# Optimization experiments

Hardware: AMD Instinct MI355X
Metric: run time of the kernel (lower is better)

## Reference

```python
import jax, jax.numpy as jnp
import numpy as np


def setup_inputs() -> dict:
    key = jax.random.key(0)
    k1, k2, k3, k4 = jax.random.split(key, 4)
    E, A = 1024, 64
    embedded = jax.random.normal(k1, (4, 4096, E), dtype=jnp.float32)
    # nn.Linear(E, A, bias=False) weight has shape [A, E]; y = x @ W.T
    W_K = jax.random.normal(k2, (A, E), dtype=jnp.float32) * (E ** -0.5)
    W_Q = jax.random.normal(k3, (A, E), dtype=jnp.float32) * (E ** -0.5)
    W_V = jax.random.normal(k4, (A, E), dtype=jnp.float32) * (E ** -0.5)
    return {"embedded": embedded, "W_K": W_K, "W_Q": W_Q, "W_V": W_V}


def reference(embedded, W_K, W_Q, W_V):
    A = W_K.shape[0]
    K = jnp.einsum('bse,ae->bsa', embedded, W_K)
    Q = jnp.einsum('bse,ae->bsa', embedded, W_Q)
    V = jnp.einsum('bse,ae->bsa', embedded, W_V)
    scores = jnp.einsum('bqa,bka->bqk', Q, K) / jnp.sqrt(jnp.float32(A))
    S = K.shape[1]
    causal = jnp.tril(jnp.ones((S, S), dtype=bool))  # True = keep
    scores = jnp.where(causal[None, :, :], scores, -jnp.inf)
    attn = jax.nn.softmax(scores, axis=2)
    out = jnp.einsum('bqk,bka->bqa', attn, V)
    return jnp.round(out, decimals=4)
```

## Files before the change

kernel.cpp:

```cpp
#include <hip/hip_runtime.h>
#include <math.h>

#define B_DIM 4
#define S_DIM 4096
#define E_DIM 1024
#define A_DIM 64
#define M_TOT (B_DIM * S_DIM)

typedef __bf16 v8bf __attribute__((ext_vector_type(8)));
typedef __bf16 v4bf __attribute__((ext_vector_type(4)));
typedef float  v4f  __attribute__((ext_vector_type(4)));

__device__ __forceinline__ v4f mfma16(v8bf a, v8bf b, v4f c) {
    return __builtin_amdgcn_mfma_f32_16x16x32_bf16(a, b, c, 0, 0, 0);
}

__device__ __forceinline__ void lds_dma16(const void* g, void* l) {
    __builtin_amdgcn_global_load_lds(
        (const __attribute__((address_space(1))) unsigned int*)g,
        (__attribute__((address_space(3))) unsigned int*)l, 16, 0, 0);
}

__global__ __launch_bounds__(256) void wconv_kernel(
    const float* __restrict__ Wk, const float* __restrict__ Wq,
    const float* __restrict__ Wv, __bf16* __restrict__ Wb)
{
    const int i = blockIdx.x * 256 + threadIdx.x;
    const int w = i >> 14;
    const int off = (i & 16383) * 4;
    const float* s = ((w == 0) ? Wk : (w == 1) ? Wq : Wv) + off;
    float4 v = *(const float4*)s;
    v4bf o;
    o[0] = (__bf16)v.x; o[1] = (__bf16)v.y; o[2] = (__bf16)v.z; o[3] = (__bf16)v.w;
    *(v4bf*)(Wb + (size_t)w * 65536 + off) = o;
}

__global__ __launch_bounds__(256) void qkv_proj_mfma(
    const float* __restrict__ X,
    const __bf16* __restrict__ Wb,
    __bf16* __restrict__ Kb,
    __bf16* __restrict__ Qb,
    __bf16* __restrict__ Vt)
{
    const int r0   = blockIdx.x * 64;
    const int w    = threadIdx.x >> 6;
    const int lane = threadIdx.x & 63;
    const int L    = lane & 15;
    const int quad = lane >> 4;
    const int cbase = w * 48;

    __shared__ __align__(16) char smem[18432 + 49152];
    __bf16* Xs = (__bf16*)smem;
    __bf16* Bs = (__bf16*)(smem + 18432);
    float (*Tv)[65] = (float(*)[65])smem;

    v4f acc[4][3];
#pragma unroll
    for (int mi = 0; mi < 4; ++mi)
#pragma unroll
        for (int nt = 0; nt < 3; ++nt) acc[mi][nt] = (v4f){0.f, 0.f, 0.f, 0.f};

    const int brow_l  = lane >> 3;
    const int bchunk  = lane & 7;
    const int bgchunk = bchunk ^ brow_l;
    auto stageB = [&](int kc, int buf) {
#pragma unroll
        for (int j = 0; j < 6; ++j) {
            const int rowbase = w * 48 + j * 8;
            const __bf16* g = Wb + (size_t)(rowbase + brow_l) * E_DIM
                              + kc * 64 + bgchunk * 8;
            lds_dma16(g, Bs + buf * 12288 + rowbase * 64);
        }
    };

    const int xrow_i = (lane >> 4);
    const int xcol   = (lane & 15) * 4;
    float4 xr[4];
    auto loadX = [&](int kc) {
#pragma unroll
        for (int i = 0; i < 4; ++i) {
            const int row = i * 16 + w * 4 + xrow_i;
            xr[i] = *(const float4*)(X + (size_t)(r0 + row) * E_DIM + kc * 64 + xcol);
        }
    };
    auto flushX = [&](int buf) {
#pragma unroll
        for (int i = 0; i < 4; ++i) {
            const int row = i * 16 + w * 4 + xrow_i;
            v4bf o;
            o[0] = (__bf16)xr[i].x; o[1] = (__bf16)xr[i].y;
            o[2] = (__bf16)xr[i].z; o[3] = (__bf16)xr[i].w;
            *(v4bf*)(Xs + buf * 4608 + row * 72 + xcol) = o;
        }
    };

    stageB(0, 0);
    loadX(0);
    flushX(0);
    __syncthreads();

#pragma unroll 1
    for (int kc = 0; kc < 16; ++kc) {
        const int cur = kc & 1;
        if (kc < 15) {
            stageB(kc + 1, cur ^ 1);
            loadX(kc + 1);
        }
        v8bf afr[4][2];
#pragma unroll
        for (int mi = 0; mi < 4; ++mi)
#pragma unroll
            for (int ka = 0; ka < 2; ++ka)
                afr[mi][ka] = *(const v8bf*)(Xs + cur * 4608 +
                                (mi * 16 + L) * 72 + ka * 32 + quad * 8);
        v8bf bfr[3][2];
#pragma unroll
        for (int nt = 0; nt < 3; ++nt)
#pragma unroll
            for (int ka = 0; ka < 2; ++ka) {
                const int R = cbase + nt * 16 + L;
                const int slot = (ka * 4 + quad) ^ (R & 7);
                bfr[nt][ka] = *(const v8bf*)(Bs + cur * 12288 + R * 64 + slot * 8);
            }
#pragma unroll
        for (int mi = 0; mi < 4; ++mi)
#pragma unroll
            for (int nt = 0; nt < 3; ++nt)
#pragma unroll
                for (int ka = 0; ka < 2; ++ka)
                    acc[mi][nt] = mfma16(afr[mi][ka], bfr[nt][ka], acc[mi][nt]);

        if (kc < 15) flushX(cur ^ 1);
        __syncthreads();
    }

#pragma unroll
    for (int nt = 0; nt < 3; ++nt) {
        const int c0 = cbase + nt * 16;
        if (c0 < 64) {
#pragma unroll
            for (int mi = 0; mi < 4; ++mi)
#pragma unroll
                for (int r = 0; r < 4; ++r)
                    Kb[(size_t)(r0 + mi * 16 + quad * 4 + r) * A_DIM + c0 + L] =
                        (__bf16)acc[mi][nt][r];
        } else if (c0 < 128) {
#pragma unroll
            for (int mi = 0; mi < 4; ++mi)
#pragma unroll
                for (int r = 0; r < 4; ++r)
                    Qb[(size_t)(r0 + mi * 16 + quad * 4 + r) * A_DIM + (c0 - 64) + L] =
                        (__bf16)(acc[mi][nt][r] * 0.125f);
        } else {
#pragma unroll
            for (int mi = 0; mi < 4; ++mi)
#pragma unroll
                for (int r = 0; r < 4; ++r)
                    Tv[mi * 16 + quad * 4 + r][(c0 - 128) + L] = acc[mi][nt][r];
        }
    }
    __syncthreads();

    {
        const int batch = r0 >> 12;
        const int s0    = r0 & 4095;
        const int a     = threadIdx.x >> 2;
        const int part  = threadIdx.x & 3;
        __bf16* vrow = Vt + (size_t)(batch * 64 + a) * S_DIM + s0 + part * 16;
#pragma unroll
        for (int h = 0; h < 2; ++h) {
            v8bf pk;
#pragma unroll
            for (int j = 0; j < 8; ++j)
                pk[j] = (__bf16)Tv[part * 16 + h * 8 + j][a];
            *(v8bf*)(vrow + h * 8) = pk;
        }
    }
}

__global__ __launch_bounds__(512, 2) void attn_fused(
    const __bf16* __restrict__ Qb,
    const __bf16* __restrict__ Kb,
    const __bf16* __restrict__ Vt,
    float* __restrict__ out)
{
    const int b  = blockIdx.y;
    const int qt = blockIdx.x;

    const int w    = threadIdx.x >> 6;
    const int lane = threadIdx.x & 63;
    const int L    = lane & 15;
    const int quad = lane >> 4;

    __shared__ __align__(16) char smem[73728];
    __bf16 (*Pt)[64][72]   = (__bf16(*)[64][72])smem;
    float*  red_l          = (float*)smem;
    float (*red_o)[64][65] = (float(*)[64][65])(smem + 2048);
    float*  invs           = (float*)(smem + 2048 + 66560);

    v8bf qf[4][2];
#pragma unroll
    for (int ni = 0; ni < 4; ++ni)
#pragma unroll
        for (int ka = 0; ka < 2; ++ka)
            qf[ni][ka] = *(const v8bf*)(Qb +
                (size_t)(b * S_DIM + qt * 64 + ni * 16 + L) * A_DIM + ka * 32 + quad * 8);

    v4f acc_o[4][4];
#pragma unroll
    for (int i = 0; i < 4; ++i)
#pragma unroll
        for (int j = 0; j < 4; ++j) acc_o[i][j] = (v4f){0.f, 0.f, 0.f, 0.f};
    float lrun[4] = {0.f, 0.f, 0.f, 0.f};

    for (int kt = w; kt <= qt; kt += 8) {
        v8bf kf[4][2];
#pragma unroll
        for (int mi = 0; mi < 4; ++mi)
#pragma unroll
            for (int ka = 0; ka < 2; ++ka)
                kf[mi][ka] = *(const v8bf*)(Kb +
                    (size_t)(b * S_DIM + kt * 64 + mi * 16 + L) * A_DIM + ka * 32 + quad * 8);
        v8bf vf[4][2];
#pragma unroll
        for (int ma = 0; ma < 4; ++ma)
#pragma unroll
            for (int ki = 0; ki < 2; ++ki)
                vf[ma][ki] = *(const v8bf*)(Vt +
                    (size_t)(b * 64 + ma * 16 + L) * S_DIM + kt * 64 + ki * 32 + quad * 8);

        const bool diag = (kt == qt);

#pragma unroll
        for (int ni = 0; ni < 4; ++ni) {
            v4f s[4];
#pragma unroll
            for (int mi = 0; mi < 4; ++mi) s[mi] = (v4f){0.f, 0.f, 0.f, 0.f};
#pragma unroll
            for (int mi = 0; mi < 4; ++mi)
#pragma unroll
                for (int ka = 0; ka < 2; ++ka)
                    s[mi] = mfma16(kf[mi][ka], qf[ni][ka], s[mi]);

            float rs = 0.f;
#pragma unroll
            for (int mi = 0; mi < 4; ++mi) {
                v4bf p4;
#pragma unroll
                for (int r = 0; r < 4; ++r) {
                    const bool masked = diag && (mi * 16 + quad * 4 + r > ni * 16 + L);
                    const float p = masked ? 0.f : __expf(s[mi][r]);
                    rs += p;
                    p4[r] = (__bf16)p;
                }
                *(v4bf*)&Pt[w][ni * 16 + L][mi * 16 + quad * 4] = p4;
            }
            lrun[ni] += rs;
        }

        v8bf pf[4][2];
#pragma unroll
        for (int ni = 0; ni < 4; ++ni)
#pragma unroll
            for (int ki = 0; ki < 2; ++ki)
                pf[ni][ki] = *(const v8bf*)&Pt[w][ni * 16 + L][ki * 32 + quad * 8];
#pragma unroll
        for (int ma = 0; ma < 4; ++ma)
#pragma unroll
            for (int ni = 0; ni < 4; ++ni)
#pragma unroll
                for (int ki = 0; ki < 2; ++ki)
                    acc_o[ma][ni] = mfma16(vf[ma][ki], pf[ni][ki], acc_o[ma][ni]);
    }

#pragma unroll
    for (int ni = 0; ni < 4; ++ni) {
        lrun[ni] += __shfl_xor(lrun[ni], 16, 64);
        lrun[ni] += __shfl_xor(lrun[ni], 32, 64);
    }

    __syncthreads();

    if (quad == 0) {
#pragma unroll
        for (int ni = 0; ni < 4; ++ni)
            red_l[w * 64 + ni * 16 + L] = lrun[ni];
    }
    if (w >= 4) {
#pragma unroll
        for (int ma = 0; ma < 4; ++ma)
#pragma unroll
            for (int ni = 0; ni < 4; ++ni)
#pragma unroll
                for (int r = 0; r < 4; ++r)
                    red_o[w - 4][ma * 16 + quad * 4 + r][ni * 16 + L] = acc_o[ma][ni][r];
    }
    __syncthreads();

    if (w < 4) {
#pragma unroll
        for (int ma = 0; ma < 4; ++ma)
#pragma unroll
            for (int ni = 0; ni < 4; ++ni)
#pragma unroll
                for (int r = 0; r < 4; ++r)
                    acc_o[ma][ni][r] += red_o[w][ma * 16 + quad * 4 + r][ni * 16 + L];
    } else if (w == 4) {
        float d = 0.f;
#pragma unroll
        for (int c = 0; c < 8; ++c) d += red_l[c * 64 + lane];
        invs[lane] = 1.0f / d;
    }
    __syncthreads();

    if (w < 4) {
#pragma unroll
        for (int ma = 0; ma < 4; ++ma)
#pragma unroll
            for (int ni = 0; ni < 4; ++ni)
#pragma unroll
                for (int r = 0; r < 4; ++r)
                    red_o[w][ma * 16 + quad * 4 + r][ni * 16 + L] = acc_o[ma][ni][r];
    }
    __syncthreads();

    {
        const int q  = threadIdx.x >> 3;
        const int ac = (threadIdx.x & 7) << 3;
        const float sc = invs[q];
        float* dst = out + (size_t)(b * S_DIM + qt * 64 + q) * A_DIM + ac;
#pragma unroll
        for (int i4 = 0; i4 < 2; ++i4) {
            float vv[4];
#pragma unroll
            for (int j = 0; j < 4; ++j) {
                const int a = ac + i4 * 4 + j;
                vv[j] = sc * (red_o[0][a][q] + red_o[1][a][q]
                            + red_o[2][a][q] + red_o[3][a][q]);
            }
            *(float4*)(dst + i4 * 4) = make_float4(vv[0], vv[1], vv[2], vv[3]);
        }
    }
}

extern "C" void kernel_launch(void* const* d_in, const int* in_sizes, int n_in,
                              void* d_out, int out_size, void* d_ws, size_t ws_size,
                              hipStream_t stream)
{
    const float* X  = (const float*)d_in[0];
    const float* Wk = (const float*)d_in[1];
    const float* Wq = (const float*)d_in[2];
    const float* Wv = (const float*)d_in[3];
    float* out = (float*)d_out;

    __bf16* Kb = (__bf16*)d_ws;
    __bf16* Qb = Kb + (size_t)M_TOT * A_DIM;
    __bf16* Vt = Qb + (size_t)M_TOT * A_DIM;
    __bf16* Wb = Vt + (size_t)M_TOT * A_DIM;

    wconv_kernel<<<192, 256, 0, stream>>>(Wk, Wq, Wv, Wb);

    qkv_proj_mfma<<<256, 256, 0, stream>>>(X, Wb, Kb, Qb, Vt);

    dim3 g2(64, B_DIM), b2(512);
    attn_fused<<<g2, b2, 0, stream>>>(Qb, Kb, Vt, out);
}
```

Measured before the change: 146.2 us.

## Balance causal attention work by pairing half query tiles; deepen X prefetch

```diff
diff --git a/kernel.cpp b/kernel.cpp
--- a/kernel.cpp
+++ b/kernel.cpp
@@ -75,37 +75,36 @@
 
     const int xrow_i = (lane >> 4);
     const int xcol   = (lane & 15) * 4;
-    float4 xr[4];
-    auto loadX = [&](int kc) {
+    float4 xr[2][4];
+    auto loadX = [&](int kc, int set) {
 #pragma unroll
         for (int i = 0; i < 4; ++i) {
             const int row = i * 16 + w * 4 + xrow_i;
-            xr[i] = *(const float4*)(X + (size_t)(r0 + row) * E_DIM + kc * 64 + xcol);
+            xr[set][i] = *(const float4*)(X + (size_t)(r0 + row) * E_DIM + kc * 64 + xcol);
         }
     };
-    auto flushX = [&](int buf) {
+    auto flushX = [&](int set, int buf) {
 #pragma unroll
         for (int i = 0; i < 4; ++i) {
             const int row = i * 16 + w * 4 + xrow_i;
             v4bf o;
-            o[0] = (__bf16)xr[i].x; o[1] = (__bf16)xr[i].y;
-            o[2] = (__bf16)xr[i].z; o[3] = (__bf16)xr[i].w;
+            o[0] = (__bf16)xr[set][i].x; o[1] = (__bf16)xr[set][i].y;
+            o[2] = (__bf16)xr[set][i].z; o[3] = (__bf16)xr[set][i].w;
             *(v4bf*)(Xs + buf * 4608 + row * 72 + xcol) = o;
         }
     };
 
     stageB(0, 0);
-    loadX(0);
-    flushX(0);
+    loadX(0, 0);
+    loadX(1, 1);
+    flushX(0, 0);
     __syncthreads();
 
 #pragma unroll 1
     for (int kc = 0; kc < 16; ++kc) {
         const int cur = kc & 1;
-        if (kc < 15) {
-            stageB(kc + 1, cur ^ 1);
-            loadX(kc + 1);
-        }
+        if (kc < 15) stageB(kc + 1, cur ^ 1);
+        if (kc < 14) loadX(kc + 2, cur);
         v8bf afr[4][2];
 #pragma unroll
         for (int mi = 0; mi < 4; ++mi)
@@ -122,6 +121,7 @@
                 const int slot = (ka * 4 + quad) ^ (R & 7);
                 bfr[nt][ka] = *(const v8bf*)(Bs + cur * 12288 + R * 64 + slot * 8);
             }
+        if (kc < 15) flushX((kc + 1) & 1, cur ^ 1);
 #pragma unroll
         for (int mi = 0; mi < 4; ++mi)
 #pragma unroll
@@ -130,7 +130,6 @@
                 for (int ka = 0; ka < 2; ++ka)
                     acc[mi][nt] = mfma16(afr[mi][ka], bfr[nt][ka], acc[mi][nt]);
 
-        if (kc < 15) flushX(cur ^ 1);
         __syncthreads();
     }
 
@@ -184,163 +183,177 @@
     const __bf16* __restrict__ Vt,
     float* __restrict__ out)
 {
-    const int b  = blockIdx.y;
-    const int qt = blockIdx.x;
+    const int b = blockIdx.y;
+    const int p = blockIdx.x;
 
     const int w    = threadIdx.x >> 6;
     const int lane = threadIdx.x & 63;
     const int L    = lane & 15;
     const int quad = lane >> 4;
 
-    __shared__ __align__(16) char smem[73728];
-    __bf16 (*Pt)[64][72]   = (__bf16(*)[64][72])smem;
+    __shared__ __align__(16) char smem[36864];
+    __bf16 (*Pt)[32][72]   = (__bf16(*)[32][72])smem;
     float*  red_l          = (float*)smem;
-    float (*red_o)[64][65] = (float(*)[64][65])(smem + 2048);
-    float*  invs           = (float*)(smem + 2048 + 66560);
-
-    v8bf qf[4][2];
-#pragma unroll
-    for (int ni = 0; ni < 4; ++ni)
-#pragma unroll
-        for (int ka = 0; ka < 2; ++ka)
-            qf[ni][ka] = *(const v8bf*)(Qb +
-                (size_t)(b * S_DIM + qt * 64 + ni * 16 + L) * A_DIM + ka * 32 + quad * 8);
-
-    v4f acc_o[4][4];
-#pragma unroll
-    for (int i = 0; i < 4; ++i)
-#pragma unroll
-        for (int j = 0; j < 4; ++j) acc_o[i][j] = (v4f){0.f, 0.f, 0.f, 0.f};
-    float lrun[4] = {0.f, 0.f, 0.f, 0.f};
-
-    for (int kt = w; kt <= qt; kt += 8) {
-        v8bf kf[4][2];
-#pragma unroll
-        for (int mi = 0; mi < 4; ++mi)
+    float (*red_o)[64][33] = (float(*)[64][33])(smem + 1024);
+    float*  invs           = (float*)(smem + 34816);
+
+    auto phase = [&](int qt, int qoff) {
+        v8bf qf[2][2];
+#pragma unroll
+        for (int ni = 0; ni < 2; ++ni)
 #pragma unroll
             for (int ka = 0; ka < 2; ++ka)
-                kf[mi][ka] = *(const v8bf*)(Kb +
-                    (size_t)(b * S_DIM + kt * 64 + mi * 16 + L) * A_DIM + ka * 32 + quad * 8);
-        v8bf vf[4][2];
-#pragma unroll
-        for (int ma = 0; ma < 4; ++ma)
-#pragma unroll
-            for (int ki = 0; ki < 2; ++ki)
-                vf[ma][ki] = *(const v8bf*)(Vt +
-                    (size_t)(b * 64 + ma * 16 + L) * S_DIM + kt * 64 + ki * 32 + quad * 8);
-
-        const bool diag = (kt == qt);
-
-#pragma unroll
-        for (int ni = 0; ni < 4; ++ni) {
-            v4f s[4];
-#pragma unroll
-            for (int mi = 0; mi < 4; ++mi) s[mi] = (v4f){0.f, 0.f, 0.f, 0.f};
+                qf[ni][ka] = *(const v8bf*)(Qb +
+                    (size_t)(b * S_DIM + qt * 64 + qoff + ni * 16 + L) * A_DIM
+                    + ka * 32 + quad * 8);
+
+        v4f acc_o[4][2];
+#pragma unroll
+        for (int i = 0; i < 4; ++i)
+#pragma unroll
+            for (int j = 0; j < 2; ++j) acc_o[i][j] = (v4f){0.f, 0.f, 0.f, 0.f};
+        float lrun[2] = {0.f, 0.f};
+
+        for (int kt = w; kt <= qt; kt += 8) {
+            v8bf kf[4][2];
 #pragma unroll
             for (int mi = 0; mi < 4; ++mi)
 #pragma unroll
                 for (int ka = 0; ka < 2; ++ka)
-                    s[mi] = mfma16(kf[mi][ka], qf[ni][ka], s[mi]);
-
-            float rs = 0.f;
-#pragma unroll
-            for (int mi = 0; mi < 4; ++mi) {
-                v4bf p4;
-#pragma unroll
-                for (int r = 0; r < 4; ++r) {
-                    const bool masked = diag && (mi * 16 + quad * 4 + r > ni * 16 + L);
-                    const float p = masked ? 0.f : __expf(s[mi][r]);
-                    rs += p;
-                    p4[r] = (__bf16)p;
+                    kf[mi][ka] = *(const v8bf*)(Kb +
+                        (size_t)(b * S_DIM + kt * 64 + mi * 16 + L) * A_DIM
+                        + ka * 32 + quad * 8);
+            v8bf vf[4][2];
+#pragma unroll
+            for (int ma = 0; ma < 4; ++ma)
+#pragma unroll
+                for (int ki = 0; ki < 2; ++ki)
+                    vf[ma][ki] = *(const v8bf*)(Vt +
+                        (size_t)(b * 64 + ma * 16 + L) * S_DIM + kt * 64
+                        + ki * 32 + quad * 8);
+
+            const bool diag = (kt == qt);
+
+#pragma unroll
+            for (int ni = 0; ni < 2; ++ni) {
+                v4f s[4];
+#pragma unroll
+                for (int mi = 0; mi < 4; ++mi) s[mi] = (v4f){0.f, 0.f, 0.f, 0.f};
+                __builtin_amdgcn_s_setprio(1);
+#pragma unroll
+                for (int mi = 0; mi < 4; ++mi)
+#pragma unroll
+                    for (int ka = 0; ka < 2; ++ka)
+                        s[mi] = mfma16(kf[mi][ka], qf[ni][ka], s[mi]);
+                __builtin_amdgcn_s_setprio(0);
+
+                float rs = 0.f;
+#pragma unroll
+                for (int mi = 0; mi < 4; ++mi) {
+                    v4bf p4;
+#pragma unroll
+                    for (int r = 0; r < 4; ++r) {
+                        const bool masked =
+                            diag && (mi * 16 + quad * 4 + r > qoff + ni * 16 + L);
+                        const float pv = masked ? 0.f : __expf(s[mi][r]);
+                        rs += pv;
+                        p4[r] = (__bf16)pv;
+                    }
+                    *(v4bf*)&Pt[w][ni * 16 + L][mi * 16 + quad * 4] = p4;
                 }
-                *(v4bf*)&Pt[w][ni * 16 + L][mi * 16 + quad * 4] = p4;
+                lrun[ni] += rs;
             }
-            lrun[ni] += rs;
-        }
-
-        v8bf pf[4][2];
-#pragma unroll
-        for (int ni = 0; ni < 4; ++ni)
-#pragma unroll
-            for (int ki = 0; ki < 2; ++ki)
-                pf[ni][ki] = *(const v8bf*)&Pt[w][ni * 16 + L][ki * 32 + quad * 8];
-#pragma unroll
-        for (int ma = 0; ma < 4; ++ma)
-#pragma unroll
-            for (int ni = 0; ni < 4; ++ni)
+
+            v8bf pf[2][2];
+#pragma unroll
+            for (int ni = 0; ni < 2; ++ni)
 #pragma unroll
                 for (int ki = 0; ki < 2; ++ki)
-                    acc_o[ma][ni] = mfma16(vf[ma][ki], pf[ni][ki], acc_o[ma][ni]);
-    }
-
-#pragma unroll
-    for (int ni = 0; ni < 4; ++ni) {
-        lrun[ni] += __shfl_xor(lrun[ni], 16, 64);
-        lrun[ni] += __shfl_xor(lrun[ni], 32, 64);
-    }
-
-    __syncthreads();
-
-    if (quad == 0) {
-#pragma unroll
-        for (int ni = 0; ni < 4; ++ni)
-            red_l[w * 64 + ni * 16 + L] = lrun[ni];
-    }
-    if (w >= 4) {
-#pragma unroll
-        for (int ma = 0; ma < 4; ++ma)
-#pragma unroll
-            for (int ni = 0; ni < 4; ++ni)
-#pragma unroll
-                for (int r = 0; r < 4; ++r)
-                    red_o[w - 4][ma * 16 + quad * 4 + r][ni * 16 + L] = acc_o[ma][ni][r];
-    }
-    __syncthreads();
-
-    if (w < 4) {
-#pragma unroll
-        for (int ma = 0; ma < 4; ++ma)
-#pragma unroll
-            for (int ni = 0; ni < 4; ++ni)
-#pragma unroll
-                for (int r = 0; r < 4; ++r)
-                    acc_o[ma][ni][r] += red_o[w][ma * 16 + quad * 4 + r][ni * 16 + L];
-    } else if (w == 4) {
-        float d = 0.f;
-#pragma unroll
-        for (int c = 0; c < 8; ++c) d += red_l[c * 64 + lane];
-        invs[lane] = 1.0f / d;
-    }
-    __syncthreads();
-
-    if (w < 4) {
-#pragma unroll
-        for (int ma = 0; ma < 4; ++ma)
-#pragma unroll
-            for (int ni = 0; ni < 4; ++ni)
-#pragma unroll
-                for (int r = 0; r < 4; ++r)
-                    red_o[w][ma * 16 + quad * 4 + r][ni * 16 + L] = acc_o[ma][ni][r];
-    }
-    __syncthreads();
-
-    {
-        const int q  = threadIdx.x >> 3;
-        const int ac = (threadIdx.x & 7) << 3;
-        const float sc = invs[q];
-        float* dst = out + (size_t)(b * S_DIM + qt * 64 + q) * A_DIM + ac;
-#pragma unroll
-        for (int i4 = 0; i4 < 2; ++i4) {
+                    pf[ni][ki] = *(const v8bf*)&Pt[w][ni * 16 + L][ki * 32 + quad * 8];
+            __builtin_amdgcn_s_setprio(1);
+#pragma unroll
+            for (int ma = 0; ma < 4; ++ma)
+#pragma unroll
+                for (int ni = 0; ni < 2; ++ni)
+#pragma unroll
+                    for (int ki = 0; ki < 2; ++ki)
+                        acc_o[ma][ni] = mfma16(vf[ma][ki], pf[ni][ki], acc_o[ma][ni]);
+            __builtin_amdgcn_s_setprio(0);
+        }
+
+#pragma unroll
+        for (int ni = 0; ni < 2; ++ni) {
+            lrun[ni] += __shfl_xor(lrun[ni], 16, 64);
+            lrun[ni] += __shfl_xor(lrun[ni], 32, 64);
+        }
+
+        __syncthreads();
+
+        if (quad == 0) {
+#pragma unroll
+            for (int ni = 0; ni < 2; ++ni)
+                red_l[w * 32 + ni * 16 + L] = lrun[ni];
+        }
+        if (w >= 4) {
+#pragma unroll
+            for (int ma = 0; ma < 4; ++ma)
+#pragma unroll
+                for (int ni = 0; ni < 2; ++ni)
+#pragma unroll
+                    for (int r = 0; r < 4; ++r)
+                        red_o[w - 4][ma * 16 + quad * 4 + r][ni * 16 + L] =
+                            acc_o[ma][ni][r];
+        }
+        __syncthreads();
+
+        if (w < 4) {
+#pragma unroll
+            for (int ma = 0; ma < 4; ++ma)
+#pragma unroll
+                for (int ni = 0; ni < 2; ++ni)
+#pragma unroll
+                    for (int r = 0; r < 4; ++r)
+                        acc_o[ma][ni][r] +=
+                            red_o[w][ma * 16 + quad * 4 + r][ni * 16 + L];
+        } else if (w == 4 && lane < 32) {
+            float d = 0.f;
+#pragma unroll
+            for (int c = 0; c < 8; ++c) d += red_l[c * 32 + lane];
+            invs[lane] = 1.0f / d;
+        }
+        __syncthreads();
+
+        if (w < 4) {
+#pragma unroll
+            for (int ma = 0; ma < 4; ++ma)
+#pragma unroll
+                for (int ni = 0; ni < 2; ++ni)
+#pragma unroll
+                    for (int r = 0; r < 4; ++r)
+                        red_o[w][ma * 16 + quad * 4 + r][ni * 16 + L] =
+                            acc_o[ma][ni][r];
+        }
+        __syncthreads();
+
+        {
+            const int q  = threadIdx.x >> 4;
+            const int ac = (threadIdx.x & 15) << 2;
+            const float sc = invs[q];
             float vv[4];
 #pragma unroll
             for (int j = 0; j < 4; ++j) {
-                const int a = ac + i4 * 4 + j;
+                const int a = ac + j;
                 vv[j] = sc * (red_o[0][a][q] + red_o[1][a][q]
                             + red_o[2][a][q] + red_o[3][a][q]);
             }
-            *(float4*)(dst + i4 * 4) = make_float4(vv[0], vv[1], vv[2], vv[3]);
-        }
-    }
+            *(float4*)(out + (size_t)(b * S_DIM + qt * 64 + qoff + q) * A_DIM + ac)
+                = make_float4(vv[0], vv[1], vv[2], vv[3]);
+        }
+        __syncthreads();
+    };
+
+    phase(p, 0);
+    phase(63 - p, 32);
 }
 
 extern "C" void kernel_launch(void* const* d_in, const int* in_sizes, int n_in,
```

New measurement: 168.3 us. +15.1%, slower.
